# Optimization experiments

Hardware: AMD Instinct MI355X
Metric: run time of the kernel (lower is better)

Reference implementation:

```python
import jax, jax.numpy as jnp
import numpy as np

B, S, HID = 2, 2048, 2048
NH, NKV, HD = 16, 16, 128
SCALE = 1.0 / np.sqrt(HD)


def _rotate_half(x):
    x1, x2 = jnp.split(x, 2, axis=-1)
    return jnp.concatenate([-x2, x1], axis=-1)


def setup_inputs() -> dict:
    key = jax.random.key(0)
    k1, k2, k3 = jax.random.split(key, 3)
    hidden_states = jax.random.normal(k1, (B, S, HID), dtype=jnp.float32)
    # standard RoPE cos/sin tables, shape [S, HD]
    inv_freq = 1.0 / (10000.0 ** (np.arange(0, HD, 2, dtype=np.float32) / HD))
    freqs = np.outer(np.arange(S, dtype=np.float32), inv_freq)  # [S, HD/2]
    emb = np.concatenate([freqs, freqs], axis=-1)               # [S, HD]
    cos = jnp.asarray(np.cos(emb), dtype=jnp.float32)
    sin = jnp.asarray(np.sin(emb), dtype=jnp.float32)
    # torch Linear weights are [out, in]; forward computes x @ W.T
    w_qkv = jax.random.normal(k2, ((NH + 2 * NKV) * HD, HID), dtype=jnp.float32) * 0.02
    w_o = jax.random.normal(k3, (HID, NH * HD), dtype=jnp.float32) * 0.02
    return {"hidden_states": hidden_states, "cos": cos, "sin": sin,
            "w_qkv": w_qkv, "w_o": w_o}


def reference(hidden_states, cos, sin, w_qkv, w_o):
    b, s, _ = hidden_states.shape
    qkv = hidden_states @ w_qkv.T                         # [B,S,(NH+2*NKV)*HD]
    qkv = qkv.reshape(b, s, NH + 2 * NKV, HD)
    q = qkv[:, :, :NH]                                    # [B,S,NH,HD]
    k = qkv[:, :, NH:NH + NKV]                            # [B,S,NKV,HD]
    v = qkv[:, :, NH + NKV:]                              # [B,S,NKV,HD]
    # RoPE: broadcast cos/sin [S,HD] -> [1,S,1,HD]
    c = cos[None, :, None, :]
    sn = sin[None, :, None, :]
    q = q * c + _rotate_half(q) * sn
    k = k * c + _rotate_half(k) * sn
    scores = jnp.einsum("bihd,bjhd->bhij", q, k) * SCALE  # [B,H,S,S]
    attn = jax.nn.softmax(scores, axis=-1)
    out = jnp.einsum("bhij,bjhd->bihd", attn, v)          # [B,S,H,HD]
    out = out.reshape(b, s, NH * HD)
    return out @ w_o.T                                    # [B,S,HID]
```

## Files before the change

### kernel.cpp

```cpp
#include <hip/hip_runtime.h>
#include <hip/hip_bf16.h>

typedef float f32x4 __attribute__((ext_vector_type(4)));
typedef __bf16 bf16x8 __attribute__((ext_vector_type(8)));
typedef __bf16 bf16x4 __attribute__((ext_vector_type(4)));

#define S_LEN 2048
#define NHEADS 16
#define HDIM 128
#define KLOG2E (0.08838834764831845f * 1.4426950408889634f)
#define MSHIFT 2.0f

__device__ __forceinline__ void gld_lds16(const __bf16* g, __bf16* l) {
  __builtin_amdgcn_global_load_lds(
      (__attribute__((address_space(1))) void*)(void*)g,
      (__attribute__((address_space(3))) void*)l,
      16, 0, 0);
}

template <int N>
__device__ __forceinline__ void waitv() {
  if constexpr (N == 8)      asm volatile("s_waitcnt vmcnt(8)" ::: "memory");
  else if constexpr (N == 6) asm volatile("s_waitcnt vmcnt(6)" ::: "memory");
  else if constexpr (N == 4) asm volatile("s_waitcnt vmcnt(4)" ::: "memory");
  else if constexpr (N == 3) asm volatile("s_waitcnt vmcnt(3)" ::: "memory");
  else                       asm volatile("s_waitcnt vmcnt(0)" ::: "memory");
}

__global__ __launch_bounds__(256)
void cvt_all(const float* __restrict__ i0, __bf16* __restrict__ o0,
             const float* __restrict__ i1, __bf16* __restrict__ o1,
             const float* __restrict__ i2, __bf16* __restrict__ o2) {
  int i = (blockIdx.x * 256 + threadIdx.x) * 4;
  if (i >= 25165824) return;
  const float* in;
  __bf16* out;
  if (i < 8388608)       { in = i0 + i;              out = o0 + i; }
  else if (i < 20971520) { in = i1 + (i - 8388608);  out = o1 + (i - 8388608); }
  else                   { in = i2 + (i - 20971520); out = o2 + (i - 20971520); }
  float4 v = *(const float4*)in;
  bf16x4 o;
  o[0] = (__bf16)v.x; o[1] = (__bf16)v.y; o[2] = (__bf16)v.z; o[3] = (__bf16)v.w;
  *(bf16x4*)out = o;
}

template <int MREP, bool RMAP>
__device__ __forceinline__ void gemm_core(const __bf16* __restrict__ A,
                                          const __bf16* __restrict__ B,
                                          __bf16* lds, int am0, int bn0,
                                          f32x4 (&acc)[MREP][4]) {
  constexpr int K = 2048;
  constexpr int AF = MREP * 2;
  constexpr int SLOT = (AF + 16) * 512;
  constexpr int NA = AF / 8;
  constexpr int NL = NA + 2;
  const int tid = threadIdx.x;
  const int w = tid >> 6, lane = tid & 63;
  const int l15 = lane & 15;
  const int wm = w >> 2, wn = w & 3;

  const __bf16* asrc = A + (size_t)(am0 + l15) * K + (lane >> 4) * 8;
  const __bf16* bsrc = B + (size_t)(bn0 + l15) * K + (lane >> 4) * 8;

  auto stage = [&](int t) {
    __bf16* s = lds + (t & 3) * SLOT;
#pragma unroll
    for (int i = 0; i < NA; ++i) {
      const int f = w * NA + i;
      gld_lds16(asrc + (size_t)f * (16 * K) + t * 32, s + f * 512 + lane * 8);
    }
#pragma unroll
    for (int i = 0; i < 2; ++i) {
      const int g = w * 2 + i;
      gld_lds16(bsrc + (size_t)g * (16 * K) + t * 32, s + (AF + g) * 512 + lane * 8);
    }
  };

  stage(0); stage(1); stage(2);
  waitv<2 * NL>();
  __builtin_amdgcn_s_barrier();

  for (int t = 0; t < 64; ++t) {
    if (t < 61) stage(t + 3);
    const __bf16* s = lds + (t & 3) * SLOT + lane * 8;
    const __bf16* sB = s + AF * 512;
    bf16x8 bfr[4];
#pragma unroll
    for (int j = 0; j < 4; ++j) {
      const int g = RMAP ? ((wn >> 1) * 8 + (wn & 1) * 2 + (j & 1) + (j >> 1) * 4)
                         : (wn * 4 + j);
      bfr[j] = *(const bf16x8*)(sB + g * 512);
    }
#pragma unroll
    for (int half = 0; half < MREP / 4; ++half) {
      bf16x8 af[4];
#pragma unroll
      for (int i = 0; i < 4; ++i)
        af[i] = *(const bf16x8*)(s + (wm * MREP + half * 4 + i) * 512);
      __builtin_amdgcn_s_setprio(1);
#pragma unroll
      for (int i = 0; i < 4; ++i)
#pragma unroll
        for (int j = 0; j < 4; ++j)
          acc[half * 4 + i][j] = __builtin_amdgcn_mfma_f32_16x16x32_bf16(
              af[i], bfr[j], acc[half * 4 + i][j], 0, 0, 0);
      __builtin_amdgcn_s_setprio(0);
    }
    if (t < 63) {
      if (t < 61)       waitv<2 * NL>();
      else if (t == 61) waitv<NL>();
      else              waitv<0>();
      __builtin_amdgcn_s_barrier();
    }
  }
}


__global__ __launch_bounds__(512)
void gemm_bt_qkp(const __bf16* __restrict__ A, const __bf16* __restrict__ B,
                 __bf16* __restrict__ Qp, __bf16* __restrict__ Kp,
                 const float* __restrict__ cosp, const float* __restrict__ sinp) {
  __shared__ alignas(16) char smem[139264];
  const int am0 = blockIdx.y * 256;
  const int bn0 = blockIdx.x * 256;
  const int tid = threadIdx.x;
  const int w = tid >> 6, lane = tid & 63;
  const int l15 = lane & 15, quad = lane >> 4;
  const int wm = w >> 2, wn = w & 3;
  f32x4 acc[8][4] = {};
  gemm_core<8, true>(A, B, (__bf16*)smem, am0, bn0, acc);

  __syncthreads();
  float* csb = (float*)smem;
  float* snb = csb + 256 * 68;
  const int sbase = am0 & 2047;
  for (int q = tid; q < 4096; q += 512) {
    const int row = q >> 4, dq = (q & 15) * 4;
    *(float4*)(csb + row * 68 + dq) =
        *(const float4*)(cosp + (size_t)(sbase + row) * 128 + dq);
    *(float4*)(snb + row * 68 + dq) =
        *(const float4*)(sinp + (size_t)(sbase + row) * 128 + dq);
  }
  __syncthreads();

  const int head_sel = wn >> 1;
  const int hcol0 = bn0 + head_sel * 128;
  const int head = hcol0 >> 7;
  const int h = head & 15;
  __bf16* dst = (head < 16) ? Qp : Kp;
#pragma unroll
  for (int i = 0; i < 8; ++i) {
    const int row_b = am0 + wm * 128 + i * 16 + quad * 4;
    const int bidx = row_b >> 11;
    const int s = row_b & 2047;
    const int sl = wm * 128 + i * 16 + quad * 4;
    const int s16 = s >> 4;
    const int l15p0 = s & 15;
#pragma unroll
    for (int j2 = 0; j2 < 2; ++j2) {
      const int dl = (wn & 1) * 32 + j2 * 16 + l15;
      const int dh = dl + 64;
      const int kkl = dl >> 5, qpl = (dl >> 3) & 3, el = dl & 7;
      const int kkh = dh >> 5, qph = (dh >> 3) & 3, eh = dh & 7;
      const size_t base_lo =
          (((size_t)((bidx * 16 + h) * 128 + s16) * 4 + kkl) * 64 + qpl * 16 + l15p0) * 8 + el;
      const size_t base_hi =
          (((size_t)((bidx * 16 + h) * 128 + s16) * 4 + kkh) * 64 + qph * 16 + l15p0) * 8 + eh;
#pragma unroll
      for (int r = 0; r < 4; ++r) {
        const float c = csb[(sl + r) * 68 + dl];
        const float sn = snb[(sl + r) * 68 + dl];
        const float a = acc[i][j2][r], bb = acc[i][j2 + 2][r];
        dst[base_lo + (size_t)r * 8] = (__bf16)(a * c - bb * sn);
        dst[base_hi + (size_t)r * 8] = (__bf16)(bb * c + a * sn);
      }
    }
  }
}

__global__ __launch_bounds__(512)
void gemm_bt_vp(const __bf16* __restrict__ A, const __bf16* __restrict__ B,
                __bf16* __restrict__ Vp) {
  __shared__ alignas(16) __bf16 lds[4 * 24 * 512];
  const int am0 = blockIdx.y * 128;
  const int bn0 = blockIdx.x * 256;
  const int tid = threadIdx.x;
  const int w = tid >> 6, lane = tid & 63;
  const int l15 = lane & 15, quad = lane >> 4;
  const int wm = w >> 2, wn = w & 3;
  f32x4 acc[4][4] = {};
  gemm_core<4, false>(A, B, lds, am0, bn0, acc);
#pragma unroll
  for (int i = 0; i < 4; ++i) {
    const int row_b = am0 + wm * 64 + i * 16 + quad * 4;
    const int b = row_b >> 11;
    const int key0 = row_b & 2047;
    const int quadp = (key0 >> 3) & 3;
    const int kkv = key0 >> 5;
    const int e0 = key0 & 7;
#pragma unroll
    for (int j = 0; j < 4; ++j) {
      const int col = bn0 + wn * 64 + j * 16 + l15;
      const int h = col >> 7, dd = col & 127;
      const int tt = dd >> 4, l15p = dd & 15;
      bf16x4 o;
#pragma unroll
      for (int r = 0; r < 4; ++r) o[r] = (__bf16)acc[i][j][r];
      size_t addr = (((size_t)((b * 16 + h) * 8 + tt) * 64 + kkv) * 64
                     + quadp * 16 + l15p) * 8 + e0;
      *(bf16x4*)(Vp + addr) = o;
    }
  }
}

__global__ __launch_bounds__(512)
void gemm_bt_f(const __bf16* __restrict__ A, const __bf16* __restrict__ B,
               float* __restrict__ C) {
  __shared__ alignas(16) __bf16 lds[4 * 24 * 512];
  const int am0 = blockIdx.y * 128;
  const int bn0 = blockIdx.x * 256;
  const int tid = threadIdx.x;
  const int w = tid >> 6, lane = tid & 63;
  const int l15 = lane & 15, quad = lane >> 4;
  const int wm = w >> 2, wn = w & 3;
  f32x4 acc[4][4] = {};
  gemm_core<4, false>(A, B, lds, am0, bn0, acc);
#pragma unroll
  for (int i = 0; i < 4; ++i) {
    const int row_b = am0 + wm * 64 + i * 16 + quad * 4;
#pragma unroll
    for (int j = 0; j < 4; ++j) {
      const int col = bn0 + wn * 64 + j * 16 + l15;
#pragma unroll
      for (int r = 0; r < 4; ++r)
        C[(size_t)(row_b + r) * 2048 + col] = acc[i][j][r];
    }
  }
}

__global__ __launch_bounds__(256, 4)
void attn_kernel(const __bf16* __restrict__ Qp, const __bf16* __restrict__ Kp,
                 const __bf16* __restrict__ Vp, __bf16* __restrict__ O) {
  const int lid = blockIdx.x;
  const int qt = (lid >> 3) & 15;
  const int bh = (lid & 7) * 4 + (lid >> 7);
  const int b = bh >> 4, h = bh & 15;
  const int tid = threadIdx.x;
  const int w = tid >> 6;
  const int lane = tid & 63;
  const int l15 = lane & 15, quad = lane >> 4;

  __shared__ alignas(16) __bf16 Kls[2][16 * 512];
  __shared__ alignas(16) __bf16 Vls[2][16 * 512];
  __shared__ alignas(16) __bf16 Ps[4][16 * 64];

  const __bf16* qbase = Qp + (size_t)bh * 262144 + lane * 8;
  const __bf16* kbase = Kp + (size_t)bh * 262144 + lane * 8;
  const __bf16* vbase = Vp + (size_t)bh * 262144 + lane * 8;

  bf16x8 qf[2][4];
#pragma unroll
  for (int qb = 0; qb < 2; ++qb)
#pragma unroll
    for (int kk = 0; kk < 4; ++kk)
      qf[qb][kk] =
          *(const bf16x8*)(qbase + (size_t)((qt * 8 + qb * 4 + w) * 4 + kk) * 512);

  bf16x8 onesf;
#pragma unroll
  for (int e = 0; e < 8; ++e) onesf[e] = (__bf16)1.0f;

  f32x4 o_acc[2][8] = {};
  f32x4 o_sum[2] = {};

  const int swz = (l15 & 7) << 3;
  __bf16* psw = &Ps[w][l15 * 64];

  auto stage = [&](int tile) {
    __bf16* ks = &Kls[tile & 1][0];
    __bf16* vs = &Vls[tile & 1][0];
#pragma unroll
    for (int ii = 0; ii < 4; ++ii) {
      const int c = w * 4 + ii;
      gld_lds16(kbase + ((size_t)tile * 16 + c) * 512, ks + c * 512 + lane * 8);
    }
#pragma unroll
    for (int ii = 0; ii < 4; ++ii) {
      const int c = w * 4 + ii;
      gld_lds16(vbase + (size_t)((c >> 1) * 64 + tile * 2 + (c & 1)) * 512,
                vs + c * 512 + lane * 8);
    }
  };

  stage(0);
  waitv<4>();
  __builtin_amdgcn_s_barrier();

  for (int t = 0; t < 32; ++t) {
    const __bf16* ks = &Kls[t & 1][0] + lane * 8;
    const __bf16* vs = &Vls[t & 1][0] + lane * 8;

    f32x4 sc[2][4] = {};
    __builtin_amdgcn_s_setprio(1);
#pragma unroll
    for (int kk = 0; kk < 4; ++kk) {
#pragma unroll
      for (int tt = 0; tt < 4; ++tt) {
        bf16x8 kf = *(const bf16x8*)(ks + (tt * 4 + kk) * 512);
        sc[0][tt] = __builtin_amdgcn_mfma_f32_16x16x32_bf16(kf, qf[0][kk], sc[0][tt], 0, 0, 0);
        sc[1][tt] = __builtin_amdgcn_mfma_f32_16x16x32_bf16(kf, qf[1][kk], sc[1][tt], 0, 0, 0);
      }
    }
    __builtin_amdgcn_s_setprio(0);

    bf16x8 pa[2][2];
#pragma unroll
    for (int qb = 0; qb < 2; ++qb) {
#pragma unroll
      for (int tt = 0; tt < 4; ++tt) {
        bf16x4 o;
#pragma unroll
        for (int r = 0; r < 4; ++r)
          o[r] = (__bf16)exp2f(sc[qb][tt][r] * KLOG2E - MSHIFT);
        *(bf16x4*)(psw + ((tt * 16 + quad * 4) ^ swz)) = o;
      }
      pa[qb][0] = *(const bf16x8*)(psw + ((quad * 8) ^ swz));
      pa[qb][1] = *(const bf16x8*)(psw + ((32 + quad * 8) ^ swz));
    }

    waitv<0>();
    __builtin_amdgcn_s_barrier();
    if (t < 31) stage(t + 1);

    __builtin_amdgcn_s_setprio(1);
#pragma unroll
    for (int kk = 0; kk < 2; ++kk) {
      o_sum[0] = __builtin_amdgcn_mfma_f32_16x16x32_bf16(pa[0][kk], onesf, o_sum[0], 0, 0, 0);
      o_sum[1] = __builtin_amdgcn_mfma_f32_16x16x32_bf16(pa[1][kk], onesf, o_sum[1], 0, 0, 0);
#pragma unroll
      for (int tt = 0; tt < 8; ++tt) {
        bf16x8 vf = *(const bf16x8*)(vs + (tt * 2 + kk) * 512);
        o_acc[0][tt] = __builtin_amdgcn_mfma_f32_16x16x32_bf16(pa[0][kk], vf, o_acc[0][tt], 0, 0, 0);
        o_acc[1][tt] = __builtin_amdgcn_mfma_f32_16x16x32_bf16(pa[1][kk], vf, o_acc[1][tt], 0, 0, 0);
      }
    }
    __builtin_amdgcn_s_setprio(0);

    if (t < 31) {
      waitv<4>();
      __builtin_amdgcn_s_barrier();
    }
  }

#pragma unroll
  for (int qb = 0; qb < 2; ++qb) {
    float inv[4];
#pragma unroll
    for (int r = 0; r < 4; ++r) inv[r] = 1.0f / o_sum[qb][r];
    const int row0 = qt * 128 + (qb * 4 + w) * 16 + quad * 4;
#pragma unroll
    for (int tt = 0; tt < 8; ++tt)
#pragma unroll
      for (int r = 0; r < 4; ++r)
        O[(size_t)(b * S_LEN + row0 + r) * 2048 + h * HDIM + tt * 16 + l15] =
            (__bf16)(o_acc[qb][tt][r] * inv[r]);
  }
}

extern "C" void kernel_launch(void* const* d_in, const int* in_sizes, int n_in,
                              void* d_out, int out_size, void* d_ws, size_t ws_size,
                              hipStream_t stream) {
  const float* hs   = (const float*)d_in[0];
  const float* cosp = (const float*)d_in[1];
  const float* sinp = (const float*)d_in[2];
  const float* wqkv = (const float*)d_in[3];
  const float* wo   = (const float*)d_in[4];
  float* out = (float*)d_out;

  char* ws = (char*)d_ws;
  __bf16* Xb   = (__bf16*)(ws);
  __bf16* Obuf = (__bf16*)(ws);
  __bf16* Wqb  = (__bf16*)(ws + 16777216);
  __bf16* Wob  = (__bf16*)(ws + 41943040);
  __bf16* Qp   = (__bf16*)(ws + 50331648);
  __bf16* Kp   = (__bf16*)(ws + 67108864);
  __bf16* Vp   = (__bf16*)(ws + 83886080);
  if (ws_size < 100663296) return;

  cvt_all<<<24576, 256, 0, stream>>>(hs, Xb, wqkv, Wqb, wo, Wob);

  gemm_bt_qkp<<<dim3(16, 16), 512, 0, stream>>>(Xb, Wqb, Qp, Kp, cosp, sinp);
  gemm_bt_vp<<<dim3(8, 32), 512, 0, stream>>>(Xb, Wqb + 8388608, Vp);
  attn_kernel<<<512, 256, 0, stream>>>(Qp, Kp, Vp, Obuf);
  gemm_bt_f<<<dim3(8, 32), 512, 0, stream>>>(Obuf, Wob, out);
}
```

Measured before the change: 401.8 us.

## Preload K/V fragments into registers and interleave softmax exp with PV MFMAs

Result: faster. 389.6 us (-3.0%).

```diff
diff --git a/kernel.cpp b/kernel.cpp
--- a/kernel.cpp
+++ b/kernel.cpp
@@ -238,7 +238,7 @@
   }
 }
 
-__global__ __launch_bounds__(256, 4)
+__global__ __launch_bounds__(256, 2)
 void attn_kernel(const __bf16* __restrict__ Qp, const __bf16* __restrict__ Kp,
                  const __bf16* __restrict__ Vp, __bf16* __restrict__ O) {
   const int lid = blockIdx.x;
@@ -300,49 +300,80 @@
     const __bf16* ks = &Kls[t & 1][0] + lane * 8;
     const __bf16* vs = &Vls[t & 1][0] + lane * 8;
 
+    bf16x8 kf[16];
+#pragma unroll
+    for (int f = 0; f < 16; ++f)
+      kf[f] = *(const bf16x8*)(ks + f * 512);
+
     f32x4 sc[2][4] = {};
     __builtin_amdgcn_s_setprio(1);
 #pragma unroll
-    for (int kk = 0; kk < 4; ++kk) {
-#pragma unroll
-      for (int tt = 0; tt < 4; ++tt) {
-        bf16x8 kf = *(const bf16x8*)(ks + (tt * 4 + kk) * 512);
-        sc[0][tt] = __builtin_amdgcn_mfma_f32_16x16x32_bf16(kf, qf[0][kk], sc[0][tt], 0, 0, 0);
-        sc[1][tt] = __builtin_amdgcn_mfma_f32_16x16x32_bf16(kf, qf[1][kk], sc[1][tt], 0, 0, 0);
-      }
-    }
+    for (int kk = 0; kk < 4; ++kk)
+#pragma unroll
+      for (int tt = 0; tt < 4; ++tt)
+        sc[0][tt] = __builtin_amdgcn_mfma_f32_16x16x32_bf16(
+            kf[tt * 4 + kk], qf[0][kk], sc[0][tt], 0, 0, 0);
+#pragma unroll
+    for (int kk = 0; kk < 4; ++kk)
+#pragma unroll
+      for (int tt = 0; tt < 4; ++tt)
+        sc[1][tt] = __builtin_amdgcn_mfma_f32_16x16x32_bf16(
+            kf[tt * 4 + kk], qf[1][kk], sc[1][tt], 0, 0, 0);
     __builtin_amdgcn_s_setprio(0);
 
-    bf16x8 pa[2][2];
-#pragma unroll
-    for (int qb = 0; qb < 2; ++qb) {
-#pragma unroll
-      for (int tt = 0; tt < 4; ++tt) {
-        bf16x4 o;
-#pragma unroll
-        for (int r = 0; r < 4; ++r)
-          o[r] = (__bf16)exp2f(sc[qb][tt][r] * KLOG2E - MSHIFT);
-        *(bf16x4*)(psw + ((tt * 16 + quad * 4) ^ swz)) = o;
-      }
-      pa[qb][0] = *(const bf16x8*)(psw + ((quad * 8) ^ swz));
-      pa[qb][1] = *(const bf16x8*)(psw + ((32 + quad * 8) ^ swz));
-    }
+    bf16x8 pa0[2], pa1[2];
+#pragma unroll
+    for (int tt = 0; tt < 4; ++tt) {
+      bf16x4 o;
+#pragma unroll
+      for (int r = 0; r < 4; ++r)
+        o[r] = (__bf16)__builtin_amdgcn_exp2f(
+            __builtin_fmaf(sc[0][tt][r], KLOG2E, -MSHIFT));
+      *(bf16x4*)(psw + ((tt * 16 + quad * 4) ^ swz)) = o;
+    }
+    pa0[0] = *(const bf16x8*)(psw + ((quad * 8) ^ swz));
+    pa0[1] = *(const bf16x8*)(psw + ((32 + quad * 8) ^ swz));
 
     waitv<0>();
     __builtin_amdgcn_s_barrier();
     if (t < 31) stage(t + 1);
 
+    bf16x8 vf[16];
+#pragma unroll
+    for (int f = 0; f < 16; ++f)
+      vf[f] = *(const bf16x8*)(vs + f * 512);
+
     __builtin_amdgcn_s_setprio(1);
 #pragma unroll
     for (int kk = 0; kk < 2; ++kk) {
-      o_sum[0] = __builtin_amdgcn_mfma_f32_16x16x32_bf16(pa[0][kk], onesf, o_sum[0], 0, 0, 0);
-      o_sum[1] = __builtin_amdgcn_mfma_f32_16x16x32_bf16(pa[1][kk], onesf, o_sum[1], 0, 0, 0);
-#pragma unroll
-      for (int tt = 0; tt < 8; ++tt) {
-        bf16x8 vf = *(const bf16x8*)(vs + (tt * 2 + kk) * 512);
-        o_acc[0][tt] = __builtin_amdgcn_mfma_f32_16x16x32_bf16(pa[0][kk], vf, o_acc[0][tt], 0, 0, 0);
-        o_acc[1][tt] = __builtin_amdgcn_mfma_f32_16x16x32_bf16(pa[1][kk], vf, o_acc[1][tt], 0, 0, 0);
-      }
+      o_sum[0] = __builtin_amdgcn_mfma_f32_16x16x32_bf16(pa0[kk], onesf, o_sum[0], 0, 0, 0);
+#pragma unroll
+      for (int tt = 0; tt < 8; ++tt)
+        o_acc[0][tt] = __builtin_amdgcn_mfma_f32_16x16x32_bf16(
+            pa0[kk], vf[tt * 2 + kk], o_acc[0][tt], 0, 0, 0);
+    }
+    __builtin_amdgcn_s_setprio(0);
+
+#pragma unroll
+    for (int tt = 0; tt < 4; ++tt) {
+      bf16x4 o;
+#pragma unroll
+      for (int r = 0; r < 4; ++r)
+        o[r] = (__bf16)__builtin_amdgcn_exp2f(
+            __builtin_fmaf(sc[1][tt][r], KLOG2E, -MSHIFT));
+      *(bf16x4*)(psw + ((tt * 16 + quad * 4) ^ swz)) = o;
+    }
+    pa1[0] = *(const bf16x8*)(psw + ((quad * 8) ^ swz));
+    pa1[1] = *(const bf16x8*)(psw + ((32 + quad * 8) ^ swz));
+
+    __builtin_amdgcn_s_setprio(1);
+#pragma unroll
+    for (int kk = 0; kk < 2; ++kk) {
+      o_sum[1] = __builtin_amdgcn_mfma_f32_16x16x32_bf16(pa1[kk], onesf, o_sum[1], 0, 0, 0);
+#pragma unroll
+      for (int tt = 0; tt < 8; ++tt)
+        o_acc[1][tt] = __builtin_amdgcn_mfma_f32_16x16x32_bf16(
+            pa1[kk], vf[tt * 2 + kk], o_acc[1][tt], 0, 0, 0);
     }
     __builtin_amdgcn_s_setprio(0);
 
```
